# Optimization experiments

Hardware: AMD Instinct MI355X
Metric: run time of the kernel (lower is better)

Reference implementation:

```python
import jax, jax.numpy as jnp
from jax import lax
import numpy as np

B, T, H = 4096, 512, 32


def _rnn_layer(xs, h0, Wih, Whh, bih, bhh):
    # xs: [T, B, in], h0: [B, H]. torch RNN tanh: h_t = tanh(x W_ih^T + b_ih + h W_hh^T + b_hh)
    def step(h, x_t):
        h = jnp.tanh(x_t @ Wih.T + bih + h @ Whh.T + bhh)
        return h, h
    h_last, ys = lax.scan(step, h0, xs)
    return ys, h_last  # ys: [T, B, H]


def setup_inputs() -> dict:
    key = jax.random.key(0)
    ks = jax.random.split(key, 12)
    s = 0.1  # keep tanh out of saturation
    return {
        "x": jax.random.normal(ks[0], (B, T, 1), jnp.float32),
        "h_state": jnp.zeros((2, B, H), jnp.float32),
        "Wih0": jax.random.normal(ks[1], (H, 1), jnp.float32) * s,
        "Whh0": jax.random.normal(ks[2], (H, H), jnp.float32) * s,
        "bih0": jax.random.normal(ks[3], (H,), jnp.float32) * s,
        "bhh0": jax.random.normal(ks[4], (H,), jnp.float32) * s,
        "Wih1": jax.random.normal(ks[5], (H, H), jnp.float32) * s,
        "Whh1": jax.random.normal(ks[6], (H, H), jnp.float32) * s,
        "bih1": jax.random.normal(ks[7], (H,), jnp.float32) * s,
        "bhh1": jax.random.normal(ks[8], (H,), jnp.float32) * s,
        "Wfc": jax.random.normal(ks[9], (1, H), jnp.float32) * s,
        "bfc": jax.random.normal(ks[10], (1,), jnp.float32) * s,
    }


def reference(x, h_state, Wih0, Whh0, bih0, bhh0, Wih1, Whh1, bih1, bhh1, Wfc, bfc):
    xs = jnp.transpose(x, (1, 0, 2))  # time-major [T, B, 1]
    ys0, h0_last = _rnn_layer(xs, h_state[0], Wih0, Whh0, bih0, bhh0)
    ys1, h1_last = _rnn_layer(ys0, h_state[1], Wih1, Whh1, bih1, bhh1)
    last = ys1[-1]                      # [B, H] == r_out[:, -1, :]
    pred = (last @ Wfc.T + bfc)[:, 0]   # Linear(32,1) then squeeze(-1) -> [B]
    h_new = jnp.stack([h0_last, h1_last], axis=0)  # [2, B, H]
    return pred, h_new
```

## Files before the change

kernel.cpp:

```cpp
#include <hip/hip_runtime.h>

#define BB 4096
#define TT 512
#define HH 32

typedef _Float16 half8 __attribute__((ext_vector_type(8)));
typedef _Float16 h2    __attribute__((ext_vector_type(2)));
typedef float    f32x4 __attribute__((ext_vector_type(4)));

#define MFMA16F(a, b, c) __builtin_amdgcn_mfma_f32_16x16x32_f16((a), (b), (c), 0, 0, 0)

union frag_u { half8 h8; h2 p[4]; };

__device__ __forceinline__ h2 pkrtz(float a, float b) {
    auto r = __builtin_amdgcn_cvt_pkrtz(a, b);
    union { decltype(r) i; h2 o; } u;
    u.i = r;
    return u.o;
}

__device__ __forceinline__ h2 tanh_h2(h2 v) {
    const h2 LO = {(_Float16)(-2.75f), (_Float16)(-2.75f)};
    const h2 HI = {(_Float16)(2.75f), (_Float16)(2.75f)};
    const h2 C0 = {(_Float16)(0.9976293f), (_Float16)(0.9976293f)};
    const h2 C1 = {(_Float16)(-0.3098016f), (_Float16)(-0.3098016f)};
    const h2 C2 = {(_Float16)(0.0889744f), (_Float16)(0.0889744f)};
    const h2 C3 = {(_Float16)(-0.0163448f), (_Float16)(-0.0163448f)};
    const h2 C4 = {(_Float16)(0.0016113f), (_Float16)(0.0016113f)};
    const h2 C5 = {(_Float16)(-0.00006405f), (_Float16)(-0.00006405f)};
    v = __builtin_elementwise_min(v, HI);
    v = __builtin_elementwise_max(v, LO);
    h2 u = v * v;
    h2 t = __builtin_elementwise_fma(u, C5, C4);
    t = __builtin_elementwise_fma(u, t, C3);
    t = __builtin_elementwise_fma(u, t, C2);
    t = __builtin_elementwise_fma(u, t, C1);
    t = __builtin_elementwise_fma(u, t, C0);
    return v * t;
}

__global__ __launch_bounds__(64) void rnn2_mfma(
    const float* __restrict__ x,
    const float* __restrict__ hstate,
    const float* __restrict__ Wih0,
    const float* __restrict__ Whh0,
    const float* __restrict__ bih0,
    const float* __restrict__ bhh0,
    const float* __restrict__ Wih1,
    const float* __restrict__ Whh1,
    const float* __restrict__ bih1,
    const float* __restrict__ bhh1,
    const float* __restrict__ Wfc,
    const float* __restrict__ bfc,
    float* __restrict__ out)
{
    const int l = threadIdx.x;
    const int q = l >> 4;
    const int n = l & 15;
    const int b = blockIdx.x * 16 + n;

    const int r0 = 8 * (n >> 2) + (n & 3);
    half8 A0[2], A1i[2], A1h[2];
#pragma unroll
    for (int t = 0; t < 2; ++t) {
        const int row = r0 + 4 * t;
        const float* p0 = Whh0 + row * HH + q * 8;
        const float* p1 = Wih1 + row * HH + q * 8;
        const float* p2 = Whh1 + row * HH + q * 8;
        frag_u f0, f1, f2;
#pragma unroll
        for (int jj = 0; jj < 4; ++jj) {
            f0.p[jj] = h2{(_Float16)p0[2 * jj], (_Float16)p0[2 * jj + 1]};
            f1.p[jj] = h2{(_Float16)p1[2 * jj], (_Float16)p1[2 * jj + 1]};
            f2.p[jj] = h2{(_Float16)p2[2 * jj], (_Float16)p2[2 * jj + 1]};
        }
        A0[t] = f0.h8; A1i[t] = f1.h8; A1h[t] = f2.h8;
    }

    float wxs[8], b0s[8], wfc8[8];
#pragma unroll
    for (int j = 0; j < 8; ++j) {
        const int hh = 8 * q + j;
        wxs[j]  = Wih0[hh];
        b0s[j]  = bih0[hh] + bhh0[hh];
        wfc8[j] = Wfc[hh];
    }
    f32x4 c1t0, c1t1;
#pragma unroll
    for (int r = 0; r < 4; ++r) {
        c1t0[r] = bih1[8 * q + r] + bhh1[8 * q + r];
        c1t1[r] = bih1[8 * q + 4 + r] + bhh1[8 * q + 4 + r];
    }

    frag_u hb0, hb1;
    {
        const float* p0 = hstate + b * HH + 8 * q;
        const float* p1 = hstate + BB * HH + b * HH + 8 * q;
#pragma unroll
        for (int jj = 0; jj < 4; ++jj) {
            hb0.p[jj] = h2{(_Float16)p0[2 * jj], (_Float16)p0[2 * jj + 1]};
            hb1.p[jj] = h2{(_Float16)p1[2 * jj], (_Float16)p1[2 * jj + 1]};
        }
    }

    f32x4 dbp0, dbp1;

    const float4* xp = (const float4*)(x + (size_t)b * TT);
    float4 xc = xp[0];

    {
        f32x4 c00, c01;
#pragma unroll
        for (int r = 0; r < 4; ++r) {
            c00[r] = fmaf(wxs[r], xc.x, b0s[r]);
            c01[r] = fmaf(wxs[4 + r], xc.x, b0s[4 + r]);
        }
        f32x4 d00 = MFMA16F(A0[0], hb0.h8, c00);
        f32x4 d01 = MFMA16F(A0[1], hb0.h8, c01);
        dbp0 = MFMA16F(A1h[0], hb1.h8, c1t0);
        dbp1 = MFMA16F(A1h[1], hb1.h8, c1t1);
        hb0.p[0] = tanh_h2(pkrtz(d00[0], d00[1]));
        hb0.p[1] = tanh_h2(pkrtz(d00[2], d00[3]));
        hb0.p[2] = tanh_h2(pkrtz(d01[0], d01[1]));
        hb0.p[3] = tanh_h2(pkrtz(d01[2], d01[3]));
    }

#define STEP(XT)                                                              \
    {                                                                         \
        f32x4 d10 = MFMA16F(A1i[0], hb0.h8, dbp0);                            \
        f32x4 d11 = MFMA16F(A1i[1], hb0.h8, dbp1);                            \
        f32x4 c00, c01;                                                       \
        _Pragma("unroll")                                                     \
        for (int r = 0; r < 4; ++r) {                                         \
            c00[r] = fmaf(wxs[r], (XT), b0s[r]);                              \
            c01[r] = fmaf(wxs[4 + r], (XT), b0s[4 + r]);                      \
        }                                                                     \
        f32x4 d00 = MFMA16F(A0[0], hb0.h8, c00);                              \
        f32x4 d01 = MFMA16F(A0[1], hb0.h8, c01);                              \
        hb1.p[0] = tanh_h2(pkrtz(d10[0], d10[1]));                            \
        hb1.p[1] = tanh_h2(pkrtz(d10[2], d10[3]));                            \
        hb1.p[2] = tanh_h2(pkrtz(d11[0], d11[1]));                            \
        hb1.p[3] = tanh_h2(pkrtz(d11[2], d11[3]));                            \
        dbp0 = MFMA16F(A1h[0], hb1.h8, c1t0);                                 \
        dbp1 = MFMA16F(A1h[1], hb1.h8, c1t1);                                 \
        hb0.p[0] = tanh_h2(pkrtz(d00[0], d00[1]));                            \
        hb0.p[1] = tanh_h2(pkrtz(d00[2], d00[3]));                            \
        hb0.p[2] = tanh_h2(pkrtz(d01[0], d01[1]));                            \
        hb0.p[3] = tanh_h2(pkrtz(d01[2], d01[3]));                            \
    }

    for (int k = 0; k < TT / 4 - 1; ++k) {
        float4 xn = xp[k + 1];
        STEP(xc.y);
        STEP(xc.z);
        STEP(xc.w);
        STEP(xn.x);
        xc = xn;
    }
    STEP(xc.y);
    STEP(xc.z);
    STEP(xc.w);

    {
        f32x4 d10 = MFMA16F(A1i[0], hb0.h8, dbp0);
        f32x4 d11 = MFMA16F(A1i[1], hb0.h8, dbp1);
        hb1.p[0] = tanh_h2(pkrtz(d10[0], d10[1]));
        hb1.p[1] = tanh_h2(pkrtz(d10[2], d10[3]));
        hb1.p[2] = tanh_h2(pkrtz(d11[0], d11[1]));
        hb1.p[3] = tanh_h2(pkrtz(d11[2], d11[3]));
    }

    float hf0[8], hf1[8];
#pragma unroll
    for (int jj = 0; jj < 4; ++jj) {
        hf0[2 * jj]     = (float)hb0.p[jj].x;
        hf0[2 * jj + 1] = (float)hb0.p[jj].y;
        hf1[2 * jj]     = (float)hb1.p[jj].x;
        hf1[2 * jj + 1] = (float)hb1.p[jj].y;
    }
    float p = 0.f;
#pragma unroll
    for (int j = 0; j < 8; ++j) p = fmaf(wfc8[j], hf1[j], p);
    p += __shfl_xor(p, 16);
    p += __shfl_xor(p, 32);
    if (q == 0) out[b] = p + bfc[0];

#pragma unroll
    for (int j = 0; j < 8; ++j) {
        out[BB + b * HH + 8 * q + j]           = hf0[j];
        out[BB + BB * HH + b * HH + 8 * q + j] = hf1[j];
    }
}

extern "C" void kernel_launch(void* const* d_in, const int* in_sizes, int n_in,
                              void* d_out, int out_size, void* d_ws, size_t ws_size,
                              hipStream_t stream) {
    const float* x      = (const float*)d_in[0];
    const float* hstate = (const float*)d_in[1];
    const float* Wih0   = (const float*)d_in[2];
    const float* Whh0   = (const float*)d_in[3];
    const float* bih0   = (const float*)d_in[4];
    const float* bhh0   = (const float*)d_in[5];
    const float* Wih1   = (const float*)d_in[6];
    const float* Whh1   = (const float*)d_in[7];
    const float* bih1   = (const float*)d_in[8];
    const float* bhh1   = (const float*)d_in[9];
    const float* Wfc    = (const float*)d_in[10];
    const float* bfc    = (const float*)d_in[11];
    float* out = (float*)d_out;

    dim3 grid(BB / 16);
    dim3 block(64);
    hipLaunchKernelGGL(rnn2_mfma, grid, block, 0, stream,
                       x, hstate, Wih0, Whh0, bih0, bhh0,
                       Wih1, Whh1, bih1, bhh1, Wfc, bfc, out);
}
```

Baseline: 218.2 us.

## Interleave two batch tiles per wave and use Estrin tanh polynomial

Each 64-thread block now processes two independent 16-sample batch tiles, interleaving their MFMA and tanh chains to hide the latency of the serial recurrence. The grid is halved accordingly. The tanh polynomial is reorganised into Estrin form to shorten its dependency chain at the cost of an extra multiply. Halving the block count leaves many CUs idle on a 256-CU device, so total parallelism drops.

```diff
diff --git a/kernel.cpp b/kernel.cpp
--- a/kernel.cpp
+++ b/kernel.cpp
@@ -31,15 +31,16 @@
     v = __builtin_elementwise_min(v, HI);
     v = __builtin_elementwise_max(v, LO);
     h2 u = v * v;
-    h2 t = __builtin_elementwise_fma(u, C5, C4);
-    t = __builtin_elementwise_fma(u, t, C3);
-    t = __builtin_elementwise_fma(u, t, C2);
-    t = __builtin_elementwise_fma(u, t, C1);
-    t = __builtin_elementwise_fma(u, t, C0);
+    h2 w = u * u;
+    h2 p01 = __builtin_elementwise_fma(u, C1, C0);
+    h2 p23 = __builtin_elementwise_fma(u, C3, C2);
+    h2 p45 = __builtin_elementwise_fma(u, C5, C4);
+    h2 qq = __builtin_elementwise_fma(w, p45, p23);
+    h2 t = __builtin_elementwise_fma(w, qq, p01);
     return v * t;
 }
 
-__global__ __launch_bounds__(64) void rnn2_mfma(
+__global__ __launch_bounds__(64, 1) void rnn2_mfma(
     const float* __restrict__ x,
     const float* __restrict__ hstate,
     const float* __restrict__ Wih0,
@@ -57,7 +58,8 @@
     const int l = threadIdx.x;
     const int q = l >> 4;
     const int n = l & 15;
-    const int b = blockIdx.x * 16 + n;
+    const int ba = blockIdx.x * 32 + n;
+    const int bb = ba + 16;
 
     const int r0 = 8 * (n >> 2) + (n & 3);
     half8 A0[2], A1i[2], A1h[2];
@@ -92,103 +94,166 @@
         c1t1[r] = bih1[8 * q + 4 + r] + bhh1[8 * q + 4 + r];
     }
 
-    frag_u hb0, hb1;
-    {
-        const float* p0 = hstate + b * HH + 8 * q;
-        const float* p1 = hstate + BB * HH + b * HH + 8 * q;
-#pragma unroll
-        for (int jj = 0; jj < 4; ++jj) {
-            hb0.p[jj] = h2{(_Float16)p0[2 * jj], (_Float16)p0[2 * jj + 1]};
-            hb1.p[jj] = h2{(_Float16)p1[2 * jj], (_Float16)p1[2 * jj + 1]};
-        }
-    }
-
-    f32x4 dbp0, dbp1;
-
-    const float4* xp = (const float4*)(x + (size_t)b * TT);
-    float4 xc = xp[0];
-
-    {
-        f32x4 c00, c01;
+    frag_u hb0a, hb1a, hb0b, hb1b;
+    {
+        const float* pa0 = hstate + ba * HH + 8 * q;
+        const float* pa1 = hstate + BB * HH + ba * HH + 8 * q;
+        const float* pb0 = hstate + bb * HH + 8 * q;
+        const float* pb1 = hstate + BB * HH + bb * HH + 8 * q;
+#pragma unroll
+        for (int jj = 0; jj < 4; ++jj) {
+            hb0a.p[jj] = h2{(_Float16)pa0[2 * jj], (_Float16)pa0[2 * jj + 1]};
+            hb1a.p[jj] = h2{(_Float16)pa1[2 * jj], (_Float16)pa1[2 * jj + 1]};
+            hb0b.p[jj] = h2{(_Float16)pb0[2 * jj], (_Float16)pb0[2 * jj + 1]};
+            hb1b.p[jj] = h2{(_Float16)pb1[2 * jj], (_Float16)pb1[2 * jj + 1]};
+        }
+    }
+
+    f32x4 dbp0a, dbp1a, dbp0b, dbp1b;
+
+    const float4* xpa = (const float4*)(x + (size_t)ba * TT);
+    const float4* xpb = (const float4*)(x + (size_t)bb * TT);
+    float4 xca = xpa[0];
+    float4 xcb = xpb[0];
+
+    {
+        f32x4 c00a, c01a, c00b, c01b;
 #pragma unroll
         for (int r = 0; r < 4; ++r) {
-            c00[r] = fmaf(wxs[r], xc.x, b0s[r]);
-            c01[r] = fmaf(wxs[4 + r], xc.x, b0s[4 + r]);
-        }
-        f32x4 d00 = MFMA16F(A0[0], hb0.h8, c00);
-        f32x4 d01 = MFMA16F(A0[1], hb0.h8, c01);
-        dbp0 = MFMA16F(A1h[0], hb1.h8, c1t0);
-        dbp1 = MFMA16F(A1h[1], hb1.h8, c1t1);
-        hb0.p[0] = tanh_h2(pkrtz(d00[0], d00[1]));
-        hb0.p[1] = tanh_h2(pkrtz(d00[2], d00[3]));
-        hb0.p[2] = tanh_h2(pkrtz(d01[0], d01[1]));
-        hb0.p[3] = tanh_h2(pkrtz(d01[2], d01[3]));
-    }
-
-#define STEP(XT)                                                              \
+            c00a[r] = fmaf(wxs[r], xca.x, b0s[r]);
+            c01a[r] = fmaf(wxs[4 + r], xca.x, b0s[4 + r]);
+            c00b[r] = fmaf(wxs[r], xcb.x, b0s[r]);
+            c01b[r] = fmaf(wxs[4 + r], xcb.x, b0s[4 + r]);
+        }
+        f32x4 d00a = MFMA16F(A0[0], hb0a.h8, c00a);
+        f32x4 d00b = MFMA16F(A0[0], hb0b.h8, c00b);
+        f32x4 d01a = MFMA16F(A0[1], hb0a.h8, c01a);
+        f32x4 d01b = MFMA16F(A0[1], hb0b.h8, c01b);
+        dbp0a = MFMA16F(A1h[0], hb1a.h8, c1t0);
+        dbp0b = MFMA16F(A1h[0], hb1b.h8, c1t0);
+        dbp1a = MFMA16F(A1h[1], hb1a.h8, c1t1);
+        dbp1b = MFMA16F(A1h[1], hb1b.h8, c1t1);
+        hb0a.p[0] = tanh_h2(pkrtz(d00a[0], d00a[1]));
+        hb0a.p[1] = tanh_h2(pkrtz(d00a[2], d00a[3]));
+        hb0a.p[2] = tanh_h2(pkrtz(d01a[0], d01a[1]));
+        hb0a.p[3] = tanh_h2(pkrtz(d01a[2], d01a[3]));
+        hb0b.p[0] = tanh_h2(pkrtz(d00b[0], d00b[1]));
+        hb0b.p[1] = tanh_h2(pkrtz(d00b[2], d00b[3]));
+        hb0b.p[2] = tanh_h2(pkrtz(d01b[0], d01b[1]));
+        hb0b.p[3] = tanh_h2(pkrtz(d01b[2], d01b[3]));
+    }
+
+#define STEP2(XTA, XTB)                                                       \
     {                                                                         \
-        f32x4 d10 = MFMA16F(A1i[0], hb0.h8, dbp0);                            \
-        f32x4 d11 = MFMA16F(A1i[1], hb0.h8, dbp1);                            \
-        f32x4 c00, c01;                                                       \
+        f32x4 d10a = MFMA16F(A1i[0], hb0a.h8, dbp0a);                         \
+        f32x4 d10b = MFMA16F(A1i[0], hb0b.h8, dbp0b);                         \
+        f32x4 d11a = MFMA16F(A1i[1], hb0a.h8, dbp1a);                         \
+        f32x4 d11b = MFMA16F(A1i[1], hb0b.h8, dbp1b);                         \
+        f32x4 c00a, c01a, c00b, c01b;                                         \
         _Pragma("unroll")                                                     \
         for (int r = 0; r < 4; ++r) {                                         \
-            c00[r] = fmaf(wxs[r], (XT), b0s[r]);                              \
-            c01[r] = fmaf(wxs[4 + r], (XT), b0s[4 + r]);                      \
+            c00a[r] = fmaf(wxs[r], (XTA), b0s[r]);                            \
+            c01a[r] = fmaf(wxs[4 + r], (XTA), b0s[4 + r]);                    \
+            c00b[r] = fmaf(wxs[r], (XTB), b0s[r]);                            \
+            c01b[r] = fmaf(wxs[4 + r], (XTB), b0s[4 + r]);                    \
         }                                                                     \
-        f32x4 d00 = MFMA16F(A0[0], hb0.h8, c00);                              \
-        f32x4 d01 = MFMA16F(A0[1], hb0.h8, c01);                              \
-        hb1.p[0] = tanh_h2(pkrtz(d10[0], d10[1]));                            \
-        hb1.p[1] = tanh_h2(pkrtz(d10[2], d10[3]));                            \
-        hb1.p[2] = tanh_h2(pkrtz(d11[0], d11[1]));                            \
-        hb1.p[3] = tanh_h2(pkrtz(d11[2], d11[3]));                            \
-        dbp0 = MFMA16F(A1h[0], hb1.h8, c1t0);                                 \
-        dbp1 = MFMA16F(A1h[1], hb1.h8, c1t1);                                 \
-        hb0.p[0] = tanh_h2(pkrtz(d00[0], d00[1]));                            \
-        hb0.p[1] = tanh_h2(pkrtz(d00[2], d00[3]));                            \
-        hb0.p[2] = tanh_h2(pkrtz(d01[0], d01[1]));                            \
-        hb0.p[3] = tanh_h2(pkrtz(d01[2], d01[3]));                            \
+        f32x4 d00a = MFMA16F(A0[0], hb0a.h8, c00a);                           \
+        f32x4 d00b = MFMA16F(A0[0], hb0b.h8, c00b);                           \
+        f32x4 d01a = MFMA16F(A0[1], hb0a.h8, c01a);                           \
+        f32x4 d01b = MFMA16F(A0[1], hb0b.h8, c01b);                           \
+        hb1a.p[0] = tanh_h2(pkrtz(d10a[0], d10a[1]));                         \
+        hb1b.p[0] = tanh_h2(pkrtz(d10b[0], d10b[1]));                         \
+        hb1a.p[1] = tanh_h2(pkrtz(d10a[2], d10a[3]));                         \
+        hb1b.p[1] = tanh_h2(pkrtz(d10b[2], d10b[3]));                         \
+        hb1a.p[2] = tanh_h2(pkrtz(d11a[0], d11a[1]));                         \
+        hb1b.p[2] = tanh_h2(pkrtz(d11b[0], d11b[1]));                         \
+        hb1a.p[3] = tanh_h2(pkrtz(d11a[2], d11a[3]));                         \
+        hb1b.p[3] = tanh_h2(pkrtz(d11b[2], d11b[3]));                         \
+        dbp0a = MFMA16F(A1h[0], hb1a.h8, c1t0);                               \
+        dbp0b = MFMA16F(A1h[0], hb1b.h8, c1t0);                               \
+        dbp1a = MFMA16F(A1h[1], hb1a.h8, c1t1);                               \
+        dbp1b = MFMA16F(A1h[1], hb1b.h8, c1t1);                               \
+        hb0a.p[0] = tanh_h2(pkrtz(d00a[0], d00a[1]));                         \
+        hb0b.p[0] = tanh_h2(pkrtz(d00b[0], d00b[1]));                         \
+        hb0a.p[1] = tanh_h2(pkrtz(d00a[2], d00a[3]));                         \
+        hb0b.p[1] = tanh_h2(pkrtz(d00b[2], d00b[3]));                         \
+        hb0a.p[2] = tanh_h2(pkrtz(d01a[0], d01a[1]));                         \
+        hb0b.p[2] = tanh_h2(pkrtz(d01b[0], d01b[1]));                         \
+        hb0a.p[3] = tanh_h2(pkrtz(d01a[2], d01a[3]));                         \
+        hb0b.p[3] = tanh_h2(pkrtz(d01b[2], d01b[3]));                         \
     }
 
     for (int k = 0; k < TT / 4 - 1; ++k) {
-        float4 xn = xp[k + 1];
-        STEP(xc.y);
-        STEP(xc.z);
-        STEP(xc.w);
-        STEP(xn.x);
-        xc = xn;
-    }
-    STEP(xc.y);
-    STEP(xc.z);
-    STEP(xc.w);
-
-    {
-        f32x4 d10 = MFMA16F(A1i[0], hb0.h8, dbp0);
-        f32x4 d11 = MFMA16F(A1i[1], hb0.h8, dbp1);
-        hb1.p[0] = tanh_h2(pkrtz(d10[0], d10[1]));
-        hb1.p[1] = tanh_h2(pkrtz(d10[2], d10[3]));
-        hb1.p[2] = tanh_h2(pkrtz(d11[0], d11[1]));
-        hb1.p[3] = tanh_h2(pkrtz(d11[2], d11[3]));
-    }
-
-    float hf0[8], hf1[8];
-#pragma unroll
-    for (int jj = 0; jj < 4; ++jj) {
-        hf0[2 * jj]     = (float)hb0.p[jj].x;
-        hf0[2 * jj + 1] = (float)hb0.p[jj].y;
-        hf1[2 * jj]     = (float)hb1.p[jj].x;
-        hf1[2 * jj + 1] = (float)hb1.p[jj].y;
-    }
-    float p = 0.f;
-#pragma unroll
-    for (int j = 0; j < 8; ++j) p = fmaf(wfc8[j], hf1[j], p);
-    p += __shfl_xor(p, 16);
-    p += __shfl_xor(p, 32);
-    if (q == 0) out[b] = p + bfc[0];
-
-#pragma unroll
-    for (int j = 0; j < 8; ++j) {
-        out[BB + b * HH + 8 * q + j]           = hf0[j];
-        out[BB + BB * HH + b * HH + 8 * q + j] = hf1[j];
+        float4 xna = xpa[k + 1];
+        float4 xnb = xpb[k + 1];
+        STEP2(xca.y, xcb.y);
+        STEP2(xca.z, xcb.z);
+        STEP2(xca.w, xcb.w);
+        STEP2(xna.x, xnb.x);
+        xca = xna;
+        xcb = xnb;
+    }
+    STEP2(xca.y, xcb.y);
+    STEP2(xca.z, xcb.z);
+    STEP2(xca.w, xcb.w);
+
+    {
+        f32x4 d10a = MFMA16F(A1i[0], hb0a.h8, dbp0a);
+        f32x4 d10b = MFMA16F(A1i[0], hb0b.h8, dbp0b);
+        f32x4 d11a = MFMA16F(A1i[1], hb0a.h8, dbp1a);
+        f32x4 d11b = MFMA16F(A1i[1], hb0b.h8, dbp1b);
+        hb1a.p[0] = tanh_h2(pkrtz(d10a[0], d10a[1]));
+        hb1a.p[1] = tanh_h2(pkrtz(d10a[2], d10a[3]));
+        hb1a.p[2] = tanh_h2(pkrtz(d11a[0], d11a[1]));
+        hb1a.p[3] = tanh_h2(pkrtz(d11a[2], d11a[3]));
+        hb1b.p[0] = tanh_h2(pkrtz(d10b[0], d10b[1]));
+        hb1b.p[1] = tanh_h2(pkrtz(d10b[2], d10b[3]));
+        hb1b.p[2] = tanh_h2(pkrtz(d11b[0], d11b[1]));
+        hb1b.p[3] = tanh_h2(pkrtz(d11b[2], d11b[3]));
+    }
+
+    const float bfc0 = bfc[0];
+    {
+        float hf0[8], hf1[8];
+#pragma unroll
+        for (int jj = 0; jj < 4; ++jj) {
+            hf0[2 * jj]     = (float)hb0a.p[jj].x;
+            hf0[2 * jj + 1] = (float)hb0a.p[jj].y;
+            hf1[2 * jj]     = (float)hb1a.p[jj].x;
+            hf1[2 * jj + 1] = (float)hb1a.p[jj].y;
+        }
+        float p = 0.f;
+#pragma unroll
+        for (int j = 0; j < 8; ++j) p = fmaf(wfc8[j], hf1[j], p);
+        p += __shfl_xor(p, 16);
+        p += __shfl_xor(p, 32);
+        if (q == 0) out[ba] = p + bfc0;
+#pragma unroll
+        for (int j = 0; j < 8; ++j) {
+            out[BB + ba * HH + 8 * q + j]           = hf0[j];
+            out[BB + BB * HH + ba * HH + 8 * q + j] = hf1[j];
+        }
+    }
+    {
+        float hf0[8], hf1[8];
+#pragma unroll
+        for (int jj = 0; jj < 4; ++jj) {
+            hf0[2 * jj]     = (float)hb0b.p[jj].x;
+            hf0[2 * jj + 1] = (float)hb0b.p[jj].y;
+            hf1[2 * jj]     = (float)hb1b.p[jj].x;
+            hf1[2 * jj + 1] = (float)hb1b.p[jj].y;
+        }
+        float p = 0.f;
+#pragma unroll
+        for (int j = 0; j < 8; ++j) p = fmaf(wfc8[j], hf1[j], p);
+        p += __shfl_xor(p, 16);
+        p += __shfl_xor(p, 32);
+        if (q == 0) out[bb] = p + bfc0;
+#pragma unroll
+        for (int j = 0; j < 8; ++j) {
+            out[BB + bb * HH + 8 * q + j]           = hf0[j];
+            out[BB + BB * HH + bb * HH + 8 * q + j] = hf1[j];
+        }
     }
 }
 
@@ -209,7 +274,7 @@
     const float* bfc    = (const float*)d_in[11];
     float* out = (float*)d_out;
 
-    dim3 grid(BB / 16);
+    dim3 grid(BB / 32);
     dim3 block(64);
     hipLaunchKernelGGL(rnn2_mfma, grid, block, 0, stream,
                        x, hstate, Wih0, Whh0, bih0, bhh0,
```

After: 387.3 us. 77.5% more time.
